# Optimization experiments

Measured on AMD Instinct MI355X. Metric: run time of the kernel, lower is better.

The kernel has to match this reference:

```python
import jax, jax.numpy as jnp
import numpy as np

# --- config constants (from init_kwargs) ---
ALPHA = 0.05; SIGMA = 0.2; THETA = 0.3; A = 0.02; B_PAR = 0.1; RHO = 0.5
MULT = 2.0          # config.x_range_final[1]
GAMMA = 0.5         # power-utility exponent: u(x,r)=r*x^g/g, ux=r*x^(g-1)
N_STEPS = 100; T_FINAL = 1.0; DT = T_FINAL / N_STEPS
HID = 64; BATCH = 16384
PEN_SCALE = 100.0; LOWER = 1e-6


def _mlp(W1, b1, W2, b2, W3, b3, s):
    # tiny FeedForwardSubNet: 3 -> HID -> HID -> 1, tanh activations
    h = jnp.tanh(s @ W1 + b1)
    h = jnp.tanh(h @ W2 + b2)
    return h @ W3 + b3


def _penalise(v):
    # penalise_range(v, lower): quadratic hinge below `lower`
    return PEN_SCALE * jnp.square(jnp.maximum(LOWER - v, 0.0))


def setup_inputs() -> dict:
    key = jax.random.key(0)
    ks = jax.random.split(key, 16)
    dw = jax.random.normal(ks[0], (BATCH, 1, N_STEPS), dtype=jnp.float32) * float(np.sqrt(DT))
    X0 = jnp.ones((1,), jnp.float32)
    R0 = jnp.ones((1,), jnp.float32)
    def w(k, shape, fan):
        return jax.random.normal(k, shape, jnp.float32) / np.float32(np.sqrt(fan))
    inp = {"dw": dw, "X0": X0, "R0": R0,
           "pW1": w(ks[1], (3, HID), 3), "pb1": jnp.zeros((HID,), jnp.float32),
           "pW2": w(ks[2], (HID, HID), HID), "pb2": jnp.zeros((HID,), jnp.float32),
           "pW3": w(ks[3], (HID, 1), HID), "pb3": jnp.zeros((1,), jnp.float32),
           "qW1": w(ks[4], (3, HID), 3), "qb1": jnp.zeros((HID,), jnp.float32),
           "qW2": w(ks[5], (HID, HID), HID), "qb2": jnp.zeros((HID,), jnp.float32),
           "qW3": w(ks[6], (HID, 1), HID), "qb3": jnp.zeros((1,), jnp.float32)}
    return inp


def reference(dw, X0, R0, pW1, pb1, pW2, pb2, pW3, pb3, qW1, qb1, qW2, qb2, qW3, qb3):
    Bn = dw.shape[0]
    ones = jnp.ones((Bn, 1), dw.dtype)
    times = jnp.arange(N_STEPS + 1, dtype=dw.dtype) * DT   # [N+1]
    x0 = ones * X0
    R0v = ones * R0
    b_eff = float(np.sign(RHO)) * B_PAR

    # p_0 and dp_0 = d p_0 / d x (per-sample, rowwise independent net)
    def p_of_x(xx):
        st = jnp.concatenate([MULT * times[0] * ones, xx, R0v], 1)
        return _mlp(pW1, pb1, pW2, pb2, pW3, pb3, st)
    p0, p_vjp = jax.vjp(p_of_x, x0)
    (dp0,) = p_vjp(jnp.ones_like(p0))
    pi0 = _mlp(qW1, qb1, qW2, qb2, qW3, qb3,
               jnp.concatenate([MULT * times[0] * ones, x0, R0v], 1))

    dw_t = jnp.transpose(dw, (2, 0, 1))          # [N, B, 1]
    upd = jnp.arange(N_STEPS) < (N_STEPS - 1)    # pi not updated at last step

    def step(carry, inp):
        x, min_x, W, pi = carry
        dwi, t_next, u = inp
        x = x + x * ALPHA * DT + pi * SIGMA * THETA * DT + pi * SIGMA * dwi
        min_x = jnp.minimum(x, min_x)
        W = W + dwi
        Rv = R0v * jnp.exp((A - 0.5 * b_eff ** 2) * t_next + b_eff * W)
        p = p0 * jnp.exp(-(ALPHA + 0.5 * THETA ** 2) * t_next - THETA * W)
        st = jnp.concatenate([MULT * t_next * jnp.ones_like(x), x, Rv], 1)
        pi_new = _mlp(qW1, qb1, qW2, qb2, qW3, qb3, st)
        pi = jnp.where(u, pi_new, pi)
        return (x, min_x, W, pi), (x, Rv, pi, -p)

    (xf, min_x, Wf, pif), (xs, Rs, pis, dMs) = jax.lax.scan(
        step, (x0, x0, jnp.zeros_like(x0), pi0), (dw_t, times[1:], upd))

    # stacked process data, matching tf.concat-over-axis-0 ordering: [(N+1)*B, 1]
    x_all  = jnp.concatenate([x0[None], xs], 0).reshape(-1, 1)
    r_all  = jnp.concatenate([R0v[None], Rs], 0).reshape(-1, 1)
    pi_all = jnp.concatenate([pi0[None], pis], 0).reshape(-1, 1)
    dM_all = jnp.concatenate([(-p0)[None], dMs], 0).reshape(-1, 1)
    dM2_all = jnp.tile(-dp0, (N_STEPS + 1, 1))
    proc = jnp.concatenate([x_all, r_all, pi_all, dM_all, dM2_all], 1)  # [(N+1)*B, 5]

    # losses (non_concave = False branch)
    p_fin = -dMs[-1]
    R_fin = Rs[-1]
    xc = jnp.maximum(xf, LOWER)
    ux = R_fin * xc ** (GAMMA - 1.0)
    u_val = R_fin * xc ** GAMMA / GAMMA
    pen = _penalise(min_x)
    loss_p = jnp.mean(jnp.square(p_fin + ux) + pen)
    loss_pi = loss_p + jnp.mean(-u_val + pen)

    return jnp.concatenate([proc.reshape(-1), jnp.stack([loss_p, loss_pi])])
```

## Files before the change

### kernel.cpp

```cpp
#include <hip/hip_runtime.h>
#include <hip/hip_bf16.h>
#include <math.h>

#define NSTEP 100
#define BATCH 16384
#define MB 16
#define NBLK (BATCH/MB)
#define NT 64

#define C_ALPHA 0.05f
#define C_SIGMA 0.2f
#define C_THETA 0.3f
#define C_DT    0.01f
#define C_LOWER 1e-6f
#define C_PEN   100.0f
#define LOG2E   1.4426950408889634f
#define TSCALE  (2.0f * LOG2E)
#define CRT ( 0.015f * C_DT * LOG2E)
#define CRW ( 0.1f * LOG2E)
#define CPT (-0.095f * C_DT * LOG2E)
#define CPW (-0.3f * LOG2E)

#define TSC   64.0f
#define TOFF  512.0f
#define TMAX  1023.999f
#define AXD   (1.0f + C_ALPHA * C_DT)
#define SIGTHDT (C_SIGMA * C_THETA * C_DT)

typedef __attribute__((ext_vector_type(8))) short bf16x8;
typedef __attribute__((ext_vector_type(4))) float f32x4;
typedef __attribute__((ext_vector_type(4), aligned(4))) float f32x4a;

__device__ __forceinline__ float tanh_pre(float zs) {
    float e = __builtin_amdgcn_exp2f(zs);
    return 1.0f - 2.0f * __builtin_amdgcn_rcpf(e + 1.0f);
}
__device__ __forceinline__ unsigned f2bf_u(float f) {
    unsigned u = __float_as_uint(f);
    return (u + 0x7FFFu + ((u >> 16) & 1u)) >> 16;
}
__device__ __forceinline__ unsigned pack_bf16(float a, float b) {
    union { __hip_bfloat162 h; unsigned u; } cv;
    cv.h = __float22bfloat162_rn(make_float2(a, b));
    return cv.u;
}
__device__ __forceinline__ float dpp_row_sum16(float v) {
    int t;
    t = __builtin_amdgcn_update_dpp(0, __float_as_int(v), 0x128, 0xF, 0xF, true);
    v += __int_as_float(t);
    t = __builtin_amdgcn_update_dpp(0, __float_as_int(v), 0x124, 0xF, 0xF, true);
    v += __int_as_float(t);
    t = __builtin_amdgcn_update_dpp(0, __float_as_int(v), 0x122, 0xF, 0xF, true);
    v += __int_as_float(t);
    t = __builtin_amdgcn_update_dpp(0, __float_as_int(v), 0x121, 0xF, 0xF, true);
    v += __int_as_float(t);
    return v;
}

__global__ __launch_bounds__(NT, 1) void fused_kernel(
        const float* __restrict__ dw, const float* __restrict__ X0,
        const float* __restrict__ R0,
        const float* __restrict__ pW1, const float* __restrict__ pb1,
        const float* __restrict__ pW2, const float* __restrict__ pb2,
        const float* __restrict__ pW3, const float* __restrict__ pb3,
        const float* __restrict__ qW1, const float* __restrict__ qb1,
        const float* __restrict__ qW2, const float* __restrict__ qb2,
        const float* __restrict__ qW3, const float* __restrict__ qb3,
        float* __restrict__ ws, float* __restrict__ out) {
    __shared__ __align__(16) unsigned short sW2T[64 * 72];
    __shared__ __align__(16) float sdw[MB * NSTEP];
    __shared__ __align__(16) float2 sTab[1024];

    const int tid = threadIdx.x;
    const int lane = tid;
    const int b0 = blockIdx.x * MB;
    const int l15 = lane & 15, quad = lane >> 4;

    {
        const float4* g = (const float4*)(dw + (size_t)b0 * NSTEP);
        float4* s = (float4*)sdw;
        for (int u = tid; u < MB * NSTEP / 4; u += NT) s[u] = g[u];
    }
    for (int u4 = tid; u4 < 1024; u4 += NT) {
        float4 w = ((const float4*)qW2)[u4];
        int base = u4 * 4;
        int k = base >> 6, n = base & 63;
        sW2T[(n + 0) * 72 + k] = (unsigned short)f2bf_u(w.x * TSC);
        sW2T[(n + 1) * 72 + k] = (unsigned short)f2bf_u(w.y * TSC);
        sW2T[(n + 2) * 72 + k] = (unsigned short)f2bf_u(w.z * TSC);
        sW2T[(n + 3) * 72 + k] = (unsigned short)f2bf_u(w.w * TSC);
    }
    for (int u = tid; u < 1024; u += NT) {
        float z0 = (float)u * (1.0f / TSC) - 8.0f;
        float t0 = tanh_pre(TSCALE * z0);
        float t1 = tanh_pre(TSCALE * (z0 + 1.0f / TSC));
        sTab[u] = make_float2(t0, t1 - t0);
    }
    __syncthreads();

    auto tab_prep = [&](float u, float& f) -> const float2* {
        float uc = __builtin_amdgcn_fmed3f(u, 0.0f, TMAX);
        int idx = (int)uc;
        f = uc - (float)idx;
        return &sTab[idx];
    };

    bf16x8 Bf[4][2];
    #pragma unroll
    for (int nt = 0; nt < 4; nt++) {
        const unsigned short* rp = &sW2T[(nt * 16 + l15) * 72 + quad * 8];
        Bf[nt][0] = *(const bf16x8*)rp;
        Bf[nt][1] = *(const bf16x8*)(rp + 32);
    }
    float tco[16], w1xs[16], w1rs[16], b1s[16];
    {
        const int kq = quad * 8;
        #pragma unroll
        for (int j = 0; j < 8; j++) {
            tco[j]      = qW1[kq + j]        * (2.0f * C_DT * TSC);
            tco[8 + j]  = qW1[32 + kq + j]   * (2.0f * C_DT * TSC);
            w1xs[j]     = qW1[64 + kq + j]   * TSC;
            w1xs[8 + j] = qW1[96 + kq + j]   * TSC;
            w1rs[j]     = qW1[128 + kq + j]  * TSC;
            w1rs[8 + j] = qW1[160 + kq + j]  * TSC;
            b1s[j]      = qb1[kq + j]        * TSC + TOFF;
            b1s[8 + j]  = qb1[32 + kq + j]   * TSC + TOFF;
        }
    }
    f32x4 b2a[4];
    float w3c[4][4];
    #pragma unroll
    for (int nt = 0; nt < 4; nt++) {
        #pragma unroll
        for (int r = 0; r < 4; r++) {
            b2a[nt][r] = qb2[nt * 16 + quad * 4 + r] * TSC + TOFF;
            w3c[nt][r] = qW3[nt * 16 + quad * 4 + r];
        }
    }
    const float b3 = qb3[0];
    const float X0v = X0[0], R0s = R0[0];

    float p0, dp0;
    {
        float pre = fmaf(pW1[64 + lane], X0v, fmaf(pW1[128 + lane], R0s, pb1[lane]));
        float h1 = tanh_pre(TSCALE * pre);
        float d1 = (1.0f - h1 * h1) * pW1[64 + lane];
        float a0 = pb2[lane], a1 = 0.f, a2 = 0.f, a3 = 0.f;
        float e0 = 0.f, e1 = 0.f, e2 = 0.f, e3 = 0.f;
        for (int i2 = 0; i2 < 64; i2 += 4) {
            float w0 = pW2[(i2 + 0) * 64 + lane];
            float w1 = pW2[(i2 + 1) * 64 + lane];
            float w2 = pW2[(i2 + 2) * 64 + lane];
            float w3 = pW2[(i2 + 3) * 64 + lane];
            a0 = fmaf(__shfl(h1, i2 + 0), w0, a0); e0 = fmaf(__shfl(d1, i2 + 0), w0, e0);
            a1 = fmaf(__shfl(h1, i2 + 1), w1, a1); e1 = fmaf(__shfl(d1, i2 + 1), w1, e1);
            a2 = fmaf(__shfl(h1, i2 + 2), w2, a2); e2 = fmaf(__shfl(d1, i2 + 2), w2, e2);
            a3 = fmaf(__shfl(h1, i2 + 3), w3, a3); e3 = fmaf(__shfl(d1, i2 + 3), w3, e3);
        }
        float pre2 = (a0 + a1) + (a2 + a3);
        float dpre2 = (e0 + e1) + (e2 + e3);
        float h2 = tanh_pre(TSCALE * pre2);
        float d2 = (1.0f - h2 * h2) * dpre2;
        float c1 = h2 * pW3[lane], c2 = d2 * pW3[lane];
        #pragma unroll
        for (int o = 1; o < 64; o <<= 1) {
            c1 += __shfl_xor(c1, o);
            c2 += __shfl_xor(c2, o);
        }
        p0 = c1 + pb3[0]; dp0 = c2;
    }
    const float mdp0 = -dp0;

    auto qnet = [&](float fi, float xv, float rv) -> float {
        float z[16], fr[16], h[16];
        const float2* qp[16];
        #pragma unroll
        for (int j = 0; j < 16; j++)
            z[j] = fmaf(w1xs[j], xv, fmaf(w1rs[j], rv, fmaf(tco[j], fi, b1s[j])));
        #pragma unroll
        for (int j = 0; j < 16; j++) qp[j] = tab_prep(z[j], fr[j]);
        float2 ev[16];
        #pragma unroll
        for (int j = 0; j < 16; j++) ev[j] = *qp[j];
        #pragma unroll
        for (int j = 0; j < 16; j++) h[j] = fmaf(fr[j], ev[j].y, ev[j].x);
        union { bf16x8 v; unsigned u[4]; } A0u, A1u;
        #pragma unroll
        for (int p = 0; p < 4; p++) {
            A0u.u[p] = pack_bf16(h[2 * p], h[2 * p + 1]);
            A1u.u[p] = pack_bf16(h[8 + 2 * p], h[8 + 2 * p + 1]);
        }
        f32x4 acc[4];
        #pragma unroll
        for (int nt = 0; nt < 4; nt++) {
            acc[nt] = b2a[nt];
            acc[nt] = __builtin_amdgcn_mfma_f32_16x16x32_bf16(Bf[nt][0], A0u.v, acc[nt], 0, 0, 0);
            acc[nt] = __builtin_amdgcn_mfma_f32_16x16x32_bf16(Bf[nt][1], A1u.v, acc[nt], 0, 0, 0);
        }
        float gfr[16], o[16];
        const float2* gp[16];
        #pragma unroll
        for (int nt = 0; nt < 4; nt++)
            #pragma unroll
            for (int r = 0; r < 4; r++)
                gp[nt * 4 + r] = tab_prep(acc[nt][r], gfr[nt * 4 + r]);
        float2 gv[16];
        #pragma unroll
        for (int j = 0; j < 16; j++) gv[j] = *gp[j];
        #pragma unroll
        for (int j = 0; j < 16; j++) o[j] = fmaf(gfr[j], gv[j].y, gv[j].x);
        float ps0 = 0.f, ps1 = 0.f, ps2 = 0.f, ps3 = 0.f;
        #pragma unroll
        for (int nt = 0; nt < 4; nt++) {
            ps0 = fmaf(o[nt * 4 + 0], w3c[nt][0], ps0);
            ps1 = fmaf(o[nt * 4 + 1], w3c[nt][1], ps1);
            ps2 = fmaf(o[nt * 4 + 2], w3c[nt][2], ps2);
            ps3 = fmaf(o[nt * 4 + 3], w3c[nt][3], ps3);
        }
        float ps = (ps0 + ps1) + (ps2 + ps3);
        ps += __shfl_xor(ps, 16);
        ps += __shfl_xor(ps, 32);
        return ps + b3;
    };

    float x = X0v, minx = X0v;
    float pi = qnet(0.0f, X0v, R0s);
    float* op = out + (size_t)(b0 + l15) * 5;
    if (quad == 0) {
        f32x4a o = {X0v, R0s, pi, -p0};
        *(f32x4a*)op = o;
    } else if (quad == 1) {
        op[4] = mdp0;
    }

    const float* sdwp = &sdw[l15 * NSTEP];
    float dwc = sdwp[0];
    float Rn  = R0s * __builtin_amdgcn_exp2f(fmaf(CRW, dwc, CRT));
    float pmn = p0  * __builtin_amdgcn_exp2f(fmaf(CPW, dwc, CPT));
    float spn = fmaf(dwc, C_SIGMA, SIGTHDT);
    sdwp += 1;
    float fc = 1.0f;

    #pragma unroll 1
    for (int i = 0; i < NSTEP - 1; i++) {
        float R = Rn, pm = pmn, sp = spn;
        float d2 = *sdwp++;
        Rn  *= __builtin_amdgcn_exp2f(fmaf(CRW, d2, CRT));
        pmn *= __builtin_amdgcn_exp2f(fmaf(CPW, d2, CPT));
        spn  = fmaf(d2, C_SIGMA, SIGTHDT);
        x = fmaf(x, AXD, pi * sp);
        minx = fminf(minx, x);
        float pin = qnet(fc, x, R);
        op += (size_t)BATCH * 5;
        if (quad == 0) {
            f32x4a o = {x, R, pin, -pm};
            *(f32x4a*)op = o;
        } else if (quad == 1) {
            op[4] = mdp0;
        }
        pi = pin;
        fc += 1.0f;
    }

    {
        x = fmaf(x, AXD, pi * spn);
        minx = fminf(minx, x);
        float Rf = Rn, pf = pmn;
        op += (size_t)BATCH * 5;
        if (quad == 0) {
            f32x4a o = {x, Rf, pi, -pf};
            *(f32x4a*)op = o;
        } else if (quad == 1) {
            op[4] = mdp0;
        }
        float xc = fmaxf(x, C_LOWER);
        float ux = Rf * rsqrtf(xc);
        float uval = 2.0f * Rf * sqrtf(xc);
        float d = fmaxf(C_LOWER - minx, 0.0f);
        float pen = C_PEN * d * d;
        float t1 = pf + ux;
        float v1 = dpp_row_sum16(t1 * t1 + pen);
        float v2 = dpp_row_sum16(-uval + pen);
        if (lane == 0) {
            atomicAdd(&ws[3], v1);
            atomicAdd(&ws[4], v2);
            __threadfence();
            int old = atomicAdd((int*)(ws + 5), 1);
            if (old == NBLK - 1) {
                float lp = atomicAdd(&ws[3], 0.0f) * (1.0f / (float)BATCH);
                float lq = atomicAdd(&ws[4], 0.0f) * (1.0f / (float)BATCH);
                out[(size_t)(NSTEP + 1) * BATCH * 5] = lp;
                out[(size_t)(NSTEP + 1) * BATCH * 5 + 1] = lp + lq;
            }
        }
    }
}

extern "C" void kernel_launch(void* const* d_in, const int* in_sizes, int n_in,
                              void* d_out, int out_size, void* d_ws, size_t ws_size,
                              hipStream_t stream) {
    const float* dw  = (const float*)d_in[0];
    const float* X0  = (const float*)d_in[1];
    const float* R0  = (const float*)d_in[2];
    const float* pW1 = (const float*)d_in[3];
    const float* pb1 = (const float*)d_in[4];
    const float* pW2 = (const float*)d_in[5];
    const float* pb2 = (const float*)d_in[6];
    const float* pW3 = (const float*)d_in[7];
    const float* pb3 = (const float*)d_in[8];
    const float* qW1 = (const float*)d_in[9];
    const float* qb1 = (const float*)d_in[10];
    const float* qW2 = (const float*)d_in[11];
    const float* qb2 = (const float*)d_in[12];
    const float* qW3 = (const float*)d_in[13];
    const float* qb3 = (const float*)d_in[14];
    float* out = (float*)d_out;
    float* ws  = (float*)d_ws;

    hipMemsetAsync(d_ws, 0, 64, stream);
    fused_kernel<<<NBLK, NT, 0, stream>>>(dw, X0, R0, pW1, pb1, pW2, pb2, pW3, pb3,
                                          qW1, qb1, qW2, qb2, qW3, qb3, ws, out);
}
```

Before: 232.8 us.

## Split q-net layer-1 across two waves and use exact tanh for layer 2

The block grows to two wavefronts. Each wave computes half of the hidden layer-1 activations through the tanh lookup table and exchanges its bf16 fragment with the other wave through double-buffered shared memory and a barrier. Both waves then run the layer-2 MFMAs redundantly. The layer-2 tanh now uses exp2/rcp directly on the pre-scaled accumulators instead of the table lookup. This shortens the per-step serial latency and adds a workgroup barrier at every time step.

```diff
diff --git a/kernel.cpp b/kernel.cpp
--- a/kernel.cpp
+++ b/kernel.cpp
@@ -6,7 +6,7 @@
 #define BATCH 16384
 #define MB 16
 #define NBLK (BATCH/MB)
-#define NT 64
+#define NT 128
 
 #define C_ALPHA 0.05f
 #define C_SIGMA 0.2f
@@ -27,6 +27,8 @@
 #define AXD   (1.0f + C_ALPHA * C_DT)
 #define SIGTHDT (C_SIGMA * C_THETA * C_DT)
 
+#define WG_BARRIER() asm volatile("s_waitcnt lgkmcnt(0)\n\ts_barrier" ::: "memory")
+
 typedef __attribute__((ext_vector_type(8))) short bf16x8;
 typedef __attribute__((ext_vector_type(4))) float f32x4;
 typedef __attribute__((ext_vector_type(4), aligned(4))) float f32x4a;
@@ -57,7 +59,7 @@
     return v;
 }
 
-__global__ __launch_bounds__(NT, 1) void fused_kernel(
+__global__ __launch_bounds__(NT, 2) void fused_kernel(
         const float* __restrict__ dw, const float* __restrict__ X0,
         const float* __restrict__ R0,
         const float* __restrict__ pW1, const float* __restrict__ pb1,
@@ -70,9 +72,11 @@
     __shared__ __align__(16) unsigned short sW2T[64 * 72];
     __shared__ __align__(16) float sdw[MB * NSTEP];
     __shared__ __align__(16) float2 sTab[1024];
+    __shared__ __align__(16) uint4 sA[2][2][64];
 
     const int tid = threadIdx.x;
-    const int lane = tid;
+    const int lane = tid & 63;
+    const int wv = tid >> 6;
     const int b0 = blockIdx.x * MB;
     const int l15 = lane & 15, quad = lane >> 4;
 
@@ -85,10 +89,10 @@
         float4 w = ((const float4*)qW2)[u4];
         int base = u4 * 4;
         int k = base >> 6, n = base & 63;
-        sW2T[(n + 0) * 72 + k] = (unsigned short)f2bf_u(w.x * TSC);
-        sW2T[(n + 1) * 72 + k] = (unsigned short)f2bf_u(w.y * TSC);
-        sW2T[(n + 2) * 72 + k] = (unsigned short)f2bf_u(w.z * TSC);
-        sW2T[(n + 3) * 72 + k] = (unsigned short)f2bf_u(w.w * TSC);
+        sW2T[(n + 0) * 72 + k] = (unsigned short)f2bf_u(w.x * TSCALE);
+        sW2T[(n + 1) * 72 + k] = (unsigned short)f2bf_u(w.y * TSCALE);
+        sW2T[(n + 2) * 72 + k] = (unsigned short)f2bf_u(w.z * TSCALE);
+        sW2T[(n + 3) * 72 + k] = (unsigned short)f2bf_u(w.w * TSCALE);
     }
     for (int u = tid; u < 1024; u += NT) {
         float z0 = (float)u * (1.0f / TSC) - 8.0f;
@@ -97,13 +101,6 @@
         sTab[u] = make_float2(t0, t1 - t0);
     }
     __syncthreads();
-
-    auto tab_prep = [&](float u, float& f) -> const float2* {
-        float uc = __builtin_amdgcn_fmed3f(u, 0.0f, TMAX);
-        int idx = (int)uc;
-        f = uc - (float)idx;
-        return &sTab[idx];
-    };
 
     bf16x8 Bf[4][2];
     #pragma unroll
@@ -112,20 +109,14 @@
         Bf[nt][0] = *(const bf16x8*)rp;
         Bf[nt][1] = *(const bf16x8*)(rp + 32);
     }
-    float tco[16], w1xs[16], w1rs[16], b1s[16];
-    {
-        const int kq = quad * 8;
-        #pragma unroll
-        for (int j = 0; j < 8; j++) {
-            tco[j]      = qW1[kq + j]        * (2.0f * C_DT * TSC);
-            tco[8 + j]  = qW1[32 + kq + j]   * (2.0f * C_DT * TSC);
-            w1xs[j]     = qW1[64 + kq + j]   * TSC;
-            w1xs[8 + j] = qW1[96 + kq + j]   * TSC;
-            w1rs[j]     = qW1[128 + kq + j]  * TSC;
-            w1rs[8 + j] = qW1[160 + kq + j]  * TSC;
-            b1s[j]      = qb1[kq + j]        * TSC + TOFF;
-            b1s[8 + j]  = qb1[32 + kq + j]   * TSC + TOFF;
-        }
+    float tco[8], w1xs[8], w1rs[8], b1s[8];
+    #pragma unroll
+    for (int j = 0; j < 8; j++) {
+        int k = wv * 32 + quad * 8 + j;
+        tco[j]  = qW1[k] * (2.0f * C_DT * TSC);
+        w1xs[j] = qW1[64 + k] * TSC;
+        w1rs[j] = qW1[128 + k] * TSC;
+        b1s[j]  = qb1[k] * TSC + TOFF;
     }
     f32x4 b2a[4];
     float w3c[4][4];
@@ -133,12 +124,17 @@
     for (int nt = 0; nt < 4; nt++) {
         #pragma unroll
         for (int r = 0; r < 4; r++) {
-            b2a[nt][r] = qb2[nt * 16 + quad * 4 + r] * TSC + TOFF;
+            b2a[nt][r] = qb2[nt * 16 + quad * 4 + r] * TSCALE;
             w3c[nt][r] = qW3[nt * 16 + quad * 4 + r];
         }
     }
     const float b3 = qb3[0];
     const float X0v = X0[0], R0s = R0[0];
+
+    uint4*       wA0 = &sA[0][wv][lane];
+    uint4*       wA1 = &sA[1][wv][lane];
+    const uint4* oA0 = &sA[0][1 - wv][lane];
+    const uint4* oA1 = &sA[1][1 - wv][lane];
 
     float p0, dp0;
     {
@@ -171,51 +167,44 @@
     }
     const float mdp0 = -dp0;
 
-    auto qnet = [&](float fi, float xv, float rv) -> float {
-        float z[16], fr[16], h[16];
-        const float2* qp[16];
-        #pragma unroll
-        for (int j = 0; j < 16; j++)
-            z[j] = fmaf(w1xs[j], xv, fmaf(w1rs[j], rv, fmaf(tco[j], fi, b1s[j])));
-        #pragma unroll
-        for (int j = 0; j < 16; j++) qp[j] = tab_prep(z[j], fr[j]);
-        float2 ev[16];
-        #pragma unroll
-        for (int j = 0; j < 16; j++) ev[j] = *qp[j];
-        #pragma unroll
-        for (int j = 0; j < 16; j++) h[j] = fmaf(fr[j], ev[j].y, ev[j].x);
-        union { bf16x8 v; unsigned u[4]; } A0u, A1u;
-        #pragma unroll
-        for (int p = 0; p < 4; p++) {
-            A0u.u[p] = pack_bf16(h[2 * p], h[2 * p + 1]);
-            A1u.u[p] = pack_bf16(h[8 + 2 * p], h[8 + 2 * p + 1]);
-        }
-        f32x4 acc[4];
-        #pragma unroll
-        for (int nt = 0; nt < 4; nt++) {
-            acc[nt] = b2a[nt];
-            acc[nt] = __builtin_amdgcn_mfma_f32_16x16x32_bf16(Bf[nt][0], A0u.v, acc[nt], 0, 0, 0);
-            acc[nt] = __builtin_amdgcn_mfma_f32_16x16x32_bf16(Bf[nt][1], A1u.v, acc[nt], 0, 0, 0);
-        }
-        float gfr[16], o[16];
-        const float2* gp[16];
-        #pragma unroll
-        for (int nt = 0; nt < 4; nt++)
-            #pragma unroll
-            for (int r = 0; r < 4; r++)
-                gp[nt * 4 + r] = tab_prep(acc[nt][r], gfr[nt * 4 + r]);
-        float2 gv[16];
-        #pragma unroll
-        for (int j = 0; j < 16; j++) gv[j] = *gp[j];
-        #pragma unroll
-        for (int j = 0; j < 16; j++) o[j] = fmaf(gfr[j], gv[j].y, gv[j].x);
+    auto qnet = [&](float fi, float xv, float rv, uint4* wA, const uint4* oA) -> float {
+        union { uint4 u4; bf16x8 v; unsigned u[4]; } Aloc;
+        {
+            float z[8], fr[8], h[8];
+            int ix[8];
+            #pragma unroll
+            for (int j = 0; j < 8; j++)
+                z[j] = fmaf(w1xs[j], xv, fmaf(w1rs[j], rv, fmaf(tco[j], fi, b1s[j])));
+            #pragma unroll
+            for (int j = 0; j < 8; j++) {
+                float uc = __builtin_amdgcn_fmed3f(z[j], 0.0f, TMAX);
+                ix[j] = (int)uc;
+                fr[j] = uc - (float)ix[j];
+            }
+            float2 ev[8];
+            #pragma unroll
+            for (int j = 0; j < 8; j++) ev[j] = sTab[ix[j]];
+            #pragma unroll
+            for (int j = 0; j < 8; j++) h[j] = fmaf(fr[j], ev[j].y, ev[j].x);
+            #pragma unroll
+            for (int p = 0; p < 4; p++)
+                Aloc.u[p] = pack_bf16(h[2 * p], h[2 * p + 1]);
+        }
+        *wA = Aloc.u4;
+        WG_BARRIER();
+        bf16x8 Aoth = *(const bf16x8*)oA;
+        bf16x8 A0 = (wv == 0) ? Aloc.v : Aoth;
+        bf16x8 A1 = (wv == 0) ? Aoth : Aloc.v;
+        const f32x4 zero4 = {0.f, 0.f, 0.f, 0.f};
         float ps0 = 0.f, ps1 = 0.f, ps2 = 0.f, ps3 = 0.f;
         #pragma unroll
         for (int nt = 0; nt < 4; nt++) {
-            ps0 = fmaf(o[nt * 4 + 0], w3c[nt][0], ps0);
-            ps1 = fmaf(o[nt * 4 + 1], w3c[nt][1], ps1);
-            ps2 = fmaf(o[nt * 4 + 2], w3c[nt][2], ps2);
-            ps3 = fmaf(o[nt * 4 + 3], w3c[nt][3], ps3);
+            f32x4 aA = __builtin_amdgcn_mfma_f32_16x16x32_bf16(Bf[nt][0], A0, b2a[nt], 0, 0, 0);
+            f32x4 aB = __builtin_amdgcn_mfma_f32_16x16x32_bf16(Bf[nt][1], A1, zero4, 0, 0, 0);
+            ps0 = fmaf(tanh_pre(aA[0] + aB[0]), w3c[nt][0], ps0);
+            ps1 = fmaf(tanh_pre(aA[1] + aB[1]), w3c[nt][1], ps1);
+            ps2 = fmaf(tanh_pre(aA[2] + aB[2]), w3c[nt][2], ps2);
+            ps3 = fmaf(tanh_pre(aA[3] + aB[3]), w3c[nt][3], ps3);
         }
         float ps = (ps0 + ps1) + (ps2 + ps3);
         ps += __shfl_xor(ps, 16);
@@ -224,13 +213,15 @@
     };
 
     float x = X0v, minx = X0v;
-    float pi = qnet(0.0f, X0v, R0s);
+    float pi = qnet(0.0f, X0v, R0s, wA0, oA0);
     float* op = out + (size_t)(b0 + l15) * 5;
-    if (quad == 0) {
-        f32x4a o = {X0v, R0s, pi, -p0};
-        *(f32x4a*)op = o;
-    } else if (quad == 1) {
-        op[4] = mdp0;
+    if (wv == 1) {
+        if (quad == 0) {
+            f32x4a o = {X0v, R0s, pi, -p0};
+            *(f32x4a*)op = o;
+        } else if (quad == 1) {
+            op[4] = mdp0;
+        }
     }
 
     const float* sdwp = &sdw[l15 * NSTEP];
@@ -241,8 +232,7 @@
     sdwp += 1;
     float fc = 1.0f;
 
-    #pragma unroll 1
-    for (int i = 0; i < NSTEP - 1; i++) {
+    auto STEP = [&](uint4* wA, const uint4* oA) {
         float R = Rn, pm = pmn, sp = spn;
         float d2 = *sdwp++;
         Rn  *= __builtin_amdgcn_exp2f(fmaf(CRW, d2, CRT));
@@ -250,47 +240,60 @@
         spn  = fmaf(d2, C_SIGMA, SIGTHDT);
         x = fmaf(x, AXD, pi * sp);
         minx = fminf(minx, x);
-        float pin = qnet(fc, x, R);
-        op += (size_t)BATCH * 5;
-        if (quad == 0) {
-            f32x4a o = {x, R, pin, -pm};
-            *(f32x4a*)op = o;
-        } else if (quad == 1) {
-            op[4] = mdp0;
+        float pin = qnet(fc, x, R, wA, oA);
+        if (wv == 1) {
+            op += (size_t)BATCH * 5;
+            if (quad == 0) {
+                f32x4a o = {x, R, pin, -pm};
+                *(f32x4a*)op = o;
+            } else if (quad == 1) {
+                op[4] = mdp0;
+            }
         }
         pi = pin;
         fc += 1.0f;
-    }
+    };
+
+    #pragma unroll 1
+    for (int it = 0; it < 49; ++it) {
+        STEP(wA1, oA1);
+        STEP(wA0, oA0);
+    }
+    STEP(wA1, oA1);
 
     {
         x = fmaf(x, AXD, pi * spn);
         minx = fminf(minx, x);
         float Rf = Rn, pf = pmn;
-        op += (size_t)BATCH * 5;
-        if (quad == 0) {
-            f32x4a o = {x, Rf, pi, -pf};
-            *(f32x4a*)op = o;
-        } else if (quad == 1) {
-            op[4] = mdp0;
-        }
-        float xc = fmaxf(x, C_LOWER);
-        float ux = Rf * rsqrtf(xc);
-        float uval = 2.0f * Rf * sqrtf(xc);
-        float d = fmaxf(C_LOWER - minx, 0.0f);
-        float pen = C_PEN * d * d;
-        float t1 = pf + ux;
-        float v1 = dpp_row_sum16(t1 * t1 + pen);
-        float v2 = dpp_row_sum16(-uval + pen);
-        if (lane == 0) {
-            atomicAdd(&ws[3], v1);
-            atomicAdd(&ws[4], v2);
-            __threadfence();
-            int old = atomicAdd((int*)(ws + 5), 1);
-            if (old == NBLK - 1) {
-                float lp = atomicAdd(&ws[3], 0.0f) * (1.0f / (float)BATCH);
-                float lq = atomicAdd(&ws[4], 0.0f) * (1.0f / (float)BATCH);
-                out[(size_t)(NSTEP + 1) * BATCH * 5] = lp;
-                out[(size_t)(NSTEP + 1) * BATCH * 5 + 1] = lp + lq;
+        if (wv == 1) {
+            op += (size_t)BATCH * 5;
+            if (quad == 0) {
+                f32x4a o = {x, Rf, pi, -pf};
+                *(f32x4a*)op = o;
+            } else if (quad == 1) {
+                op[4] = mdp0;
+            }
+        }
+        if (wv == 0) {
+            float xc = fmaxf(x, C_LOWER);
+            float ux = Rf * rsqrtf(xc);
+            float uval = 2.0f * Rf * sqrtf(xc);
+            float d = fmaxf(C_LOWER - minx, 0.0f);
+            float pen = C_PEN * d * d;
+            float t1 = pf + ux;
+            float v1 = dpp_row_sum16(t1 * t1 + pen);
+            float v2 = dpp_row_sum16(-uval + pen);
+            if (lane == 0) {
+                atomicAdd(&ws[3], v1);
+                atomicAdd(&ws[4], v2);
+                __threadfence();
+                int old = atomicAdd((int*)(ws + 5), 1);
+                if (old == NBLK - 1) {
+                    float lp = atomicAdd(&ws[3], 0.0f) * (1.0f / (float)BATCH);
+                    float lq = atomicAdd(&ws[4], 0.0f) * (1.0f / (float)BATCH);
+                    out[(size_t)(NSTEP + 1) * BATCH * 5] = lp;
+                    out[(size_t)(NSTEP + 1) * BATCH * 5 + 1] = lp + lq;
+                }
             }
         }
     }
```

After: 228.7 us. Within noise of the previous version (-1.7%).
